# Performance work log

Hardware: AMD Instinct MI355X
Metric: run time of the kernel (lower is better)

Reference implementation:

```python
import jax, jax.numpy as jnp
import numpy as np

B, DIM, HW = 16, 256, 64      # input feature map
G, DH = 8, 64                 # offset_groups = heads = 8, dim_head = 64
DPG = DIM // G                # 32 channels per group
TP = 8                        # tile size: 8x8 grid of 8x8 tiles
DS = 4                        # downsample factor -> 2x2 offset grid per tile
CPB_DIM = DIM // 4            # 64, CPB mlp width
SCALE = DH ** -0.5


def _grid_sample(img, grid):
    # F.grid_sample, bilinear, zero padding, align_corners=False
    # img (N,C,H,W), grid (N,Ho,Wo,2) with last dim (x,y) in [-1,1]
    N, C, H, W = img.shape
    Ho, Wo = grid.shape[1:3]
    x = ((grid[..., 0] + 1.0) * W - 1.0) / 2.0
    y = ((grid[..., 1] + 1.0) * H - 1.0) / 2.0
    x0 = jnp.floor(x)
    y0 = jnp.floor(y)
    imgf = img.reshape(N, C, H * W)
    out = jnp.zeros((N, C, Ho * Wo), img.dtype)
    for dx, wx in ((0.0, x0 + 1.0 - x), (1.0, x - x0)):
        for dy, wy in ((0.0, y0 + 1.0 - y), (1.0, y - y0)):
            ix = x0 + dx
            iy = y0 + dy
            valid = (ix >= 0) & (ix < W) & (iy >= 0) & (iy < H)
            idx = (jnp.clip(iy, 0, H - 1) * W + jnp.clip(ix, 0, W - 1)).astype(jnp.int32)
            idxf = idx.reshape(N, Ho * Wo)
            g = jax.vmap(lambda im, ii: im[:, ii])(imgf, idxf)  # (N,C,HoWo)
            w = (wx * wy * valid).reshape(N, 1, Ho * Wo)
            out = out + g * w
    return out.reshape(N, C, Ho, Wo)


def _forward(x, ln_g, ln_b, wq, wk, wv, off_w1, off_b1, off_w2,
             cpb_w1, cpb_b1, cpb_w2, cpb_b2, cpb_w3, cpb_b3, wo, bo):
    Bb, C, H, W = x.shape
    # LayerNorm over channel dim (eps=1e-6)
    xt = jnp.moveaxis(x, 1, -1)
    mu = xt.mean(-1, keepdims=True)
    var = ((xt - mu) ** 2).mean(-1, keepdims=True)
    xt = (xt - mu) * jax.lax.rsqrt(var + 1e-6) * ln_g + ln_b
    x = jnp.moveaxis(xt, -1, 1)
    # patchify: (b c (i p) (j q)) -> ((i j b) c p q)  [vectorizes the 64-iter python loop]
    xp = x.reshape(Bb, C, 8, TP, 8, TP).transpose(2, 4, 0, 1, 3, 5).reshape(64 * Bb, C, TP, TP)
    N = 64 * Bb
    # grouped 1x1 to_q (groups = offset_groups)
    xg = xp.reshape(N, G, DPG, TP, TP)
    q = jnp.einsum('ngchw,goc->ngohw', xg, wq)          # (N,8,64,8,8)
    gq = q.reshape(N * G, DH, TP, TP)
    # offset net: depthwise conv k=6 s=4 p=1 -> GELU -> 1x1 -> tanh -> *offset_scale
    off = jax.lax.conv_general_dilated(gq, off_w1, (DS, DS), ((1, 1), (1, 1)),
                                       feature_group_count=DH)
    off = jax.nn.gelu(off + off_b1[None, :, None, None], approximate=False)
    off = jnp.tanh(jnp.einsum('nchw,oc->nohw', off, off_w2)) * float(DS)  # (N*G,2,2,2)
    # virtual sampling grid on the 2x2 offset grid, normalized by (size-1)
    r = jnp.arange(2, dtype=x.dtype)
    gx, gy = jnp.meshgrid(r, r, indexing='xy')
    vgrid = jnp.stack([gx, gy])[None] + off              # (N*G,2,2,2) ch=(x,y)
    vnorm = 2.0 * vgrid - 1.0                            # max(2-1,1)=1
    vgrid_s = jnp.moveaxis(vnorm, 1, -1)                 # (N*G,2,2,2) last=(x,y)
    kv = _grid_sample(xp.reshape(N * G, DPG, TP, TP), vgrid_s)   # (N*G,32,2,2)
    kvf = kv.reshape(N, G, DPG, 2, 2)
    k = jnp.einsum('ngchw,goc->ngohw', kvf, wk)          # (N,8,64,2,2)
    v = jnp.einsum('ngchw,goc->ngohw', kvf, wv)
    qh = q.transpose(0, 1, 3, 4, 2).reshape(N, G, TP * TP, DH) * SCALE
    kh = k.transpose(0, 1, 3, 4, 2).reshape(N, G, 4, DH)
    vh = v.transpose(0, 1, 3, 4, 2).reshape(N, G, 4, DH)
    sim = jnp.einsum('bhid,bhjd->bhij', qh, kh)          # (N,8,64,4)
    # continuous position bias (CPB)
    rq = jnp.arange(TP, dtype=x.dtype)
    qx, qy = jnp.meshgrid(rq, rq, indexing='xy')
    gridq = jnp.stack([qx, qy], -1).reshape(TP * TP, 2) * (2.0 / (TP - 1)) - 1.0
    pos = gridq[None, :, None, :] - vgrid_s.reshape(N * G, 1, 4, 2)  # (N*G,64,4,2)
    bz = jnp.sign(pos) * jnp.log1p(jnp.abs(pos))
    bz = jax.nn.relu(bz @ cpb_w1 + cpb_b1)
    bz = jax.nn.relu(bz @ cpb_w2 + cpb_b2)
    bz = (bz @ cpb_w3 + cpb_b3).reshape(N, G, TP * TP, 4)
    attn = jax.nn.softmax(sim + bz, axis=-1)
    out = jnp.einsum('bhij,bhjd->bhid', attn, vh)        # (N,8,64,64)
    out = out.transpose(0, 1, 3, 2).reshape(N, G * DH, TP, TP)
    out = jnp.einsum('nchw,oc->nohw', out, wo) + bo[None, :, None, None]
    # reassemble: ((i j b) c p q) -> (b c (i p) (j q))
    y = out.reshape(8, 8, Bb, C, TP, TP).transpose(2, 3, 0, 4, 1, 5).reshape(Bb, C, H, W)
    return y


def setup_inputs() -> dict:
    key = jax.random.key(0)
    ks = jax.random.split(key, 12)
    s = 0.05
    return {
        'x': jax.random.normal(ks[0], (B, DIM, HW, HW), jnp.float32),
        'ln_g': jnp.ones((DIM,), jnp.float32),
        'ln_b': jnp.zeros((DIM,), jnp.float32),
        'wq': jax.random.normal(ks[1], (G, DH, DPG), jnp.float32) * s,
        'wk': jax.random.normal(ks[2], (G, DH, DPG), jnp.float32) * s,
        'wv': jax.random.normal(ks[3], (G, DH, DPG), jnp.float32) * s,
        'off_w1': jax.random.normal(ks[4], (DH, 1, 6, 6), jnp.float32) * s,
        'off_b1': jnp.zeros((DH,), jnp.float32),
        'off_w2': jax.random.normal(ks[5], (2, DH), jnp.float32) * s,
        'cpb_w1': jax.random.normal(ks[6], (2, CPB_DIM), jnp.float32) * s,
        'cpb_b1': jnp.zeros((CPB_DIM,), jnp.float32),
        'cpb_w2': jax.random.normal(ks[7], (CPB_DIM, CPB_DIM), jnp.float32) * s,
        'cpb_b2': jnp.zeros((CPB_DIM,), jnp.float32),
        'cpb_w3': jax.random.normal(ks[8], (CPB_DIM, 1), jnp.float32) * s,
        'cpb_b3': jnp.zeros((1,), jnp.float32),
        'wo': jax.random.normal(ks[9], (DIM, G * DH), jnp.float32) * s,
        'bo': jnp.zeros((DIM,), jnp.float32),
    }


def reference(x, ln_g, ln_b, wq, wk, wv, off_w1, off_b1, off_w2,
              cpb_w1, cpb_b1, cpb_w2, cpb_b2, cpb_w3, cpb_b3, wo, bo):
    return _forward(x, ln_g, ln_b, wq, wk, wv, off_w1, off_b1, off_w2,
                    cpb_w1, cpb_b1, cpb_w2, cpb_b2, cpb_w3, cpb_b3, wo, bo)
```

## Files before the change

### kernel.cpp

```cpp
#include <hip/hip_runtime.h>
#include <math.h>


#define WS_VN  16777216
#define WS_WOT 16842752

typedef __attribute__((ext_vector_type(8))) short short8;
typedef __attribute__((ext_vector_type(4))) short short4b;
typedef __attribute__((ext_vector_type(4))) float f32x4;

__device__ __forceinline__ short f2bf(float f) {
  unsigned u = __builtin_bit_cast(unsigned, f);
  u += 0x7fff + ((u >> 16) & 1);
  return (short)(u >> 16);
}
__device__ __forceinline__ float bf2f(short h) {
  return __builtin_bit_cast(float, ((unsigned)(unsigned short)h) << 16);
}

__global__ __launch_bounds__(256) void k1_ln(const float* __restrict__ x,
    const float* __restrict__ ln_g, const float* __restrict__ ln_b,
    float* __restrict__ xn) {
  int blk = blockIdx.x;
  int b = blk >> 6, h = blk & 63;
  int t = threadIdx.x;
  int quarter = t >> 6, wcol = t & 63;
  const float* xrow = x + (size_t)b * (256 * 4096) + h * 64 + wcol;
  float vv[64];
  float s = 0.f, ss = 0.f;
#pragma unroll
  for (int i = 0; i < 64; ++i) {
    float v = xrow[(size_t)(quarter * 64 + i) * 4096];
    vv[i] = v; s += v; ss += v * v;
  }
  __shared__ float sm[4][64], sq[4][64], mu_s[64], rs_s[64];
  sm[quarter][wcol] = s; sq[quarter][wcol] = ss;
  __syncthreads();
  if (t < 64) {
    float S  = sm[0][t] + sm[1][t] + sm[2][t] + sm[3][t];
    float SS = sq[0][t] + sq[1][t] + sq[2][t] + sq[3][t];
    float mu = S * (1.f / 256.f);
    float var = SS * (1.f / 256.f) - mu * mu;
    mu_s[t] = mu;
    rs_s[t] = 1.f / sqrtf(var + 1e-6f);
  }
  __syncthreads();
  float mu = mu_s[wcol], rs = rs_s[wcol];
  int it = h >> 3, p = h & 7, jt = wcol >> 3, qq = wcol & 7;
  int n = (it * 8 + jt) * 16 + b;
  int pos = p * 8 + qq;
  float* xo = xn + (size_t)n * 16384 + pos * 256 + quarter * 64;
#pragma unroll
  for (int i = 0; i < 64; i += 4) {
    float4 o4;
    o4.x = (vv[i + 0] - mu) * rs * ln_g[quarter * 64 + i + 0] + ln_b[quarter * 64 + i + 0];
    o4.y = (vv[i + 1] - mu) * rs * ln_g[quarter * 64 + i + 1] + ln_b[quarter * 64 + i + 1];
    o4.z = (vv[i + 2] - mu) * rs * ln_g[quarter * 64 + i + 2] + ln_b[quarter * 64 + i + 2];
    o4.w = (vv[i + 3] - mu) * rs * ln_g[quarter * 64 + i + 3] + ln_b[quarter * 64 + i + 3];
    *(float4*)&xo[i] = o4;
  }
}

__global__ __launch_bounds__(256) void k0_cvt(const float* __restrict__ wo,
    short* __restrict__ woH, short* __restrict__ woL,
    const float* __restrict__ wq,
    short* __restrict__ wqH, short* __restrict__ wqL) {
  int blk = blockIdx.x;
  if (blk < 512) {
    int idx = blk * 256 + threadIdx.x;
    float v = wo[idx];
    short hi = f2bf(v);
    woH[idx] = hi;
    woL[idx] = f2bf(v - bf2f(hi));
  } else {
    int idx = (blk - 512) * 256 + threadIdx.x;
    float v = wq[idx];
    short hi = f2bf(v);
    wqH[idx] = hi;
    wqL[idx] = f2bf(v - bf2f(hi));
  }
}

__global__ __launch_bounds__(256, 4) void k2_qoff(const float* __restrict__ xn,
    const short* __restrict__ wqH, const short* __restrict__ wqL,
    const float* __restrict__ w1, const float* __restrict__ b1,
    const float* __restrict__ w2, short* __restrict__ qb,
    float* __restrict__ vn) {
  int blk = blockIdx.x;
  int n = blk >> 1, gh = blk & 1;
  int w = threadIdx.x >> 6;
  int lane = threadIdx.x & 63;
  int l15 = lane & 15, q4 = lane >> 4;
  __shared__ float qs[64][65];

  const float* w1c = w1 + lane * 36;
  float b1v = b1[lane];
  float w2a = w2[lane];
  float w2b = w2[64 + lane];
  int oy = w >> 1, ox = w & 1;
  int posc = w * 16 + l15;

  for (int gi = 0; gi < 4; ++gi) {
    int g = gh * 4 + gi;
    int ng = n * 8 + g;
    const float* xb = xn + (size_t)n * 16384 + posc * 256 + g * 32 + q4 * 8;
    float4 v0 = *(const float4*)xb;
    float4 v1 = *(const float4*)(xb + 4);
    float vj[8] = {v0.x, v0.y, v0.z, v0.w, v1.x, v1.y, v1.z, v1.w};
    short8 BH, BL;
#pragma unroll
    for (int j = 0; j < 8; ++j) {
      float v = vj[j];
      short hi = f2bf(v);
      BH[j] = hi;
      BL[j] = f2bf(v - bf2f(hi));
    }
    const short* wqHg = wqH + g * 2048;
    const short* wqLg = wqL + g * 2048;
    short* qrow = qb + ((size_t)(n * 64 + posc) * 512 + g * 64);
#pragma unroll
    for (int mt = 0; mt < 4; ++mt) {
      short8 AH = *(const short8*)&wqHg[(mt * 16 + l15) * 32 + q4 * 8];
      short8 AL = *(const short8*)&wqLg[(mt * 16 + l15) * 32 + q4 * 8];
      f32x4 acc = {0.f, 0.f, 0.f, 0.f};
      acc = __builtin_amdgcn_mfma_f32_16x16x32_bf16(AH, BH, acc, 0, 0, 0);
      acc = __builtin_amdgcn_mfma_f32_16x16x32_bf16(AL, BH, acc, 0, 0, 0);
      acc = __builtin_amdgcn_mfma_f32_16x16x32_bf16(AH, BL, acc, 0, 0, 0);
      int obase = mt * 16 + q4 * 4;
#pragma unroll
      for (int reg = 0; reg < 4; ++reg) qs[obase + reg][posc] = acc[reg];
      short4b qv;
#pragma unroll
      for (int reg = 0; reg < 4; ++reg) qv[reg] = f2bf(acc[reg]);
      *(short4b*)&qrow[obase] = qv;
    }
    __syncthreads();
    float a = 0.f;
#pragma unroll
    for (int ky = 0; ky < 6; ++ky) {
      int iy = oy * 4 - 1 + ky;
      if (iy < 0 || iy > 7) continue;
#pragma unroll
      for (int kx = 0; kx < 6; ++kx) {
        int ix = ox * 4 - 1 + kx;
        if (ix < 0 || ix > 7) continue;
        a += w1c[ky * 6 + kx] * qs[lane][iy * 8 + ix];
      }
    }
    a += b1v;
    a = 0.5f * a * (1.f + erff(a * 0.70710678118654752f));
    float p0 = w2a * a, p1 = w2b * a;
#pragma unroll
    for (int st = 1; st < 64; st <<= 1) {
      p0 += __shfl_xor(p0, st, 64);
      p1 += __shfl_xor(p1, st, 64);
    }
    if (lane == 0) {
      float offx = tanhf(p0) * 4.f;
      float offy = tanhf(p1) * 4.f;
      float2 o2;
      o2.x = 2.f * ((float)ox + offx) - 1.f;
      o2.y = 2.f * ((float)oy + offy) - 1.f;
      *(float2*)&vn[(size_t)ng * 8 + w * 2] = o2;
    }
    __syncthreads();
  }
}

__global__ __launch_bounds__(256, 3) void k3_attn(const float* __restrict__ xn,
    const float* __restrict__ wk, const float* __restrict__ wv,
    const float* __restrict__ vn,
    const float* __restrict__ cw1, const float* __restrict__ cb1,
    const float* __restrict__ cw2, const float* __restrict__ cb2,
    const float* __restrict__ cw3, const float* __restrict__ cb3,
    short* __restrict__ qattB) {
  int w = threadIdx.x >> 6;
  int lane = threadIdx.x & 63;
  int ng = blockIdx.x * 4 + w;
  int n = ng >> 3, g = ng & 7;
  __shared__ alignas(16) float kvs[4][32][4];
  __shared__ alignas(16) float ks[4][64][4];
  __shared__ alignas(16) float vs[4][64][4];
  __shared__ alignas(16) short bfragLDS[512 * 8];
  __shared__ float biasS[4][4][64];

  {
    int t = threadIdx.x;
#pragma unroll
    for (int rep = 0; rep < 2; ++rep) {
      int slot = t + rep * 256;
      int combo = slot >> 6, ln = slot & 63;
      int kstep = combo >> 2, nt = combo & 3;
      int kbase = kstep * 32 + (ln >> 4) * 8;
      int ncol = nt * 16 + (ln & 15);
      short8 v;
#pragma unroll
      for (int jj = 0; jj < 8; ++jj) v[jj] = f2bf(cw2[(kbase + jj) * 64 + ncol]);
      *(short8*)&bfragLDS[slot * 8] = v;
    }
  }

  const float* vp = vn + (size_t)ng * 8;
  float vx0 = vp[0], vy0 = vp[1], vx1 = vp[2], vy1 = vp[3];
  float vx2 = vp[4], vy2 = vp[5], vx3 = vp[6], vy3 = vp[7];
  {
    int c = lane & 31, s2 = lane >> 5;
    const float* tile = xn + (size_t)n * 16384 + g * 32 + c;
#pragma unroll
    for (int rep = 0; rep < 2; ++rep) {
      int s = s2 + 2 * rep;
      float vxs = (rep == 0) ? (s2 ? vx1 : vx0) : (s2 ? vx3 : vx2);
      float vys = (rep == 0) ? (s2 ? vy1 : vy0) : (s2 ? vy3 : vy2);
      float X = 4.f * vxs + 3.5f, Y = 4.f * vys + 3.5f;
      float x0f = floorf(X), y0f = floorf(Y);
      int x0 = (int)x0f, y0 = (int)y0f;
      float wx1 = X - x0f, wy1 = Y - y0f;
      float acc = 0.f;
      for (int dy = 0; dy < 2; ++dy) {
        int iy = y0 + dy;
        if (iy < 0 || iy > 7) continue;
        float wyv = dy ? wy1 : 1.f - wy1;
        for (int dx = 0; dx < 2; ++dx) {
          int ix = x0 + dx;
          if (ix < 0 || ix > 7) continue;
          float wxv = dx ? wx1 : 1.f - wx1;
          acc += tile[(iy * 8 + ix) * 256] * wxv * wyv;
        }
      }
      kvs[w][c][s] = acc;
    }
  }
  __syncthreads();
  {
    int d = lane;
    float ka0 = 0, ka1 = 0, ka2 = 0, ka3 = 0, va0 = 0, va1 = 0, va2 = 0, va3 = 0;
    const float4* wk4 = (const float4*)(wk + g * 2048 + d * 32);
    const float4* wv4 = (const float4*)(wv + g * 2048 + d * 32);
#pragma unroll
    for (int c4 = 0; c4 < 8; ++c4) {
      float4 a4 = wk4[c4], b4 = wv4[c4];
      float aw[4] = {a4.x, a4.y, a4.z, a4.w};
      float bw[4] = {b4.x, b4.y, b4.z, b4.w};
#pragma unroll
      for (int u = 0; u < 4; ++u) {
        float4 kv4 = *(const float4*)kvs[w][c4 * 4 + u];
        ka0 += aw[u] * kv4.x; ka1 += aw[u] * kv4.y;
        ka2 += aw[u] * kv4.z; ka3 += aw[u] * kv4.w;
        va0 += bw[u] * kv4.x; va1 += bw[u] * kv4.y;
        va2 += bw[u] * kv4.z; va3 += bw[u] * kv4.w;
      }
    }
    ks[w][d][0] = ka0; ks[w][d][1] = ka1; ks[w][d][2] = ka2; ks[w][d][3] = ka3;
    vs[w][d][0] = va0; vs[w][d][1] = va1; vs[w][d][2] = va2; vs[w][d][3] = va3;
  }
  __syncthreads();
  float sim0 = 0, sim1 = 0, sim2 = 0, sim3 = 0;
  short* qrow = qattB + ((size_t)(n * 64 + lane) * 512 + g * 64);
#pragma unroll 2
  for (int d8 = 0; d8 < 8; ++d8) {
    short8 q8 = *(const short8*)&qrow[d8 * 8];
#pragma unroll
    for (int j = 0; j < 8; ++j) {
      float qv = bf2f(q8[j]);
      float4 k4 = *(const float4*)ks[w][d8 * 8 + j];
      sim0 += qv * k4.x; sim1 += qv * k4.y; sim2 += qv * k4.z; sim3 += qv * k4.w;
    }
  }
  float logit0 = sim0 * 0.125f, logit1 = sim1 * 0.125f;
  float logit2 = sim2 * 0.125f, logit3 = sim3 * 0.125f;

  short8 bf[2][4];
#pragma unroll
  for (int kstep = 0; kstep < 2; ++kstep)
#pragma unroll
    for (int nt = 0; nt < 4; ++nt)
      bf[kstep][nt] = *(const short8*)&bfragLDS[((kstep * 4 + nt) * 64 + lane) * 8];
  int kcol = (lane >> 4) * 8;
  float c1x[16], c1y[16], c1b[16];
#pragma unroll
  for (int ks2 = 0; ks2 < 2; ++ks2)
#pragma unroll
    for (int jj = 0; jj < 8; ++jj) {
      int i = ks2 * 32 + kcol + jj;
      c1x[ks2 * 8 + jj] = cw1[i];
      c1y[ks2 * 8 + jj] = cw1[64 + i];
      c1b[ks2 * 8 + jj] = cb1[i];
    }
  int jme = lane & 15;
  float w3v[4], b2v[4];
#pragma unroll
  for (int nt = 0; nt < 4; ++nt) {
    w3v[nt] = cw3[nt * 16 + jme];
    b2v[nt] = cb2[nt * 16 + jme];
  }
  float gqx = (float)(jme & 7) * (2.f / 7.f) - 1.f;
  float yrow = (float)(jme >> 3);
#pragma unroll 1
  for (int s = 0; s < 4; ++s) {
    float vxs = (s == 0) ? vx0 : (s == 1) ? vx1 : (s == 2) ? vx2 : vx3;
    float vys = (s == 0) ? vy0 : (s == 1) ? vy1 : (s == 2) ? vy2 : vy3;
    float px = gqx - vxs;
    float tx = copysignf(log1pf(fabsf(px)), px);
    float pre[16];
#pragma unroll
    for (int t2 = 0; t2 < 16; ++t2) pre[t2] = fmaf(tx, c1x[t2], c1b[t2]);
#pragma unroll 1
    for (int mt4 = 0; mt4 < 4; ++mt4) {
      float gqy = (float)(mt4 * 2) * (2.f / 7.f) + yrow * (2.f / 7.f) - 1.f;
      float py = gqy - vys;
      float ty = copysignf(log1pf(fabsf(py)), py);
      short8 af[2];
#pragma unroll
      for (int ks2 = 0; ks2 < 2; ++ks2)
#pragma unroll
        for (int jj = 0; jj < 8; ++jj) {
          float h = fmaxf(fmaf(ty, c1y[ks2 * 8 + jj], pre[ks2 * 8 + jj]), 0.f);
          af[ks2][jj] = f2bf(h);
        }
      f32x4 a0 = {0,0,0,0}, a1 = {0,0,0,0}, a2 = {0,0,0,0}, a3 = {0,0,0,0};
      a0 = __builtin_amdgcn_mfma_f32_16x16x32_bf16(af[0], bf[0][0], a0, 0, 0, 0);
      a0 = __builtin_amdgcn_mfma_f32_16x16x32_bf16(af[1], bf[1][0], a0, 0, 0, 0);
      a1 = __builtin_amdgcn_mfma_f32_16x16x32_bf16(af[0], bf[0][1], a1, 0, 0, 0);
      a1 = __builtin_amdgcn_mfma_f32_16x16x32_bf16(af[1], bf[1][1], a1, 0, 0, 0);
      a2 = __builtin_amdgcn_mfma_f32_16x16x32_bf16(af[0], bf[0][2], a2, 0, 0, 0);
      a2 = __builtin_amdgcn_mfma_f32_16x16x32_bf16(af[1], bf[1][2], a2, 0, 0, 0);
      a3 = __builtin_amdgcn_mfma_f32_16x16x32_bf16(af[0], bf[0][3], a3, 0, 0, 0);
      a3 = __builtin_amdgcn_mfma_f32_16x16x32_bf16(af[1], bf[1][3], a3, 0, 0, 0);
      float part[4];
#pragma unroll
      for (int reg = 0; reg < 4; ++reg) {
        part[reg] = w3v[0] * fmaxf(a0[reg] + b2v[0], 0.f)
                  + w3v[1] * fmaxf(a1[reg] + b2v[1], 0.f)
                  + w3v[2] * fmaxf(a2[reg] + b2v[2], 0.f)
                  + w3v[3] * fmaxf(a3[reg] + b2v[3], 0.f);
      }
#pragma unroll
      for (int st = 1; st < 16; st <<= 1)
#pragma unroll
        for (int reg = 0; reg < 4; ++reg)
          part[reg] += __shfl_xor(part[reg], st, 64);
      if (jme == 0) {
        int posO = mt4 * 16 + (lane >> 4) * 4;
#pragma unroll
        for (int reg = 0; reg < 4; ++reg) biasS[w][s][posO + reg] = part[reg];
      }
    }
  }
  __syncthreads();
  float c3 = cb3[0];
  logit0 += biasS[w][0][lane] + c3;
  logit1 += biasS[w][1][lane] + c3;
  logit2 += biasS[w][2][lane] + c3;
  logit3 += biasS[w][3][lane] + c3;
  float m = fmaxf(fmaxf(logit0, logit1), fmaxf(logit2, logit3));
  float e0 = expf(logit0 - m), e1 = expf(logit1 - m);
  float e2 = expf(logit2 - m), e3 = expf(logit3 - m);
  float inv = 1.f / (e0 + e1 + e2 + e3);
  e0 *= inv; e1 *= inv; e2 *= inv; e3 *= inv;
#pragma unroll 2
  for (int d8 = 0; d8 < 8; ++d8) {
    short8 o8;
#pragma unroll
    for (int j = 0; j < 8; ++j) {
      float4 v4 = *(const float4*)vs[w][d8 * 8 + j];
      o8[j] = f2bf(e0 * v4.x + e1 * v4.y + e2 * v4.z + e3 * v4.w);
    }
    *(short8*)&qrow[d8 * 8] = o8;
  }
}

__global__ __launch_bounds__(256) void k4_mfma(const short* __restrict__ attB,
    const short* __restrict__ woH, const short* __restrict__ woL,
    const float* __restrict__ bo, float* __restrict__ y) {
  int blk = blockIdx.x;
  int b = blk & 15, it = (blk >> 4) & 7, p = blk >> 7;
  int wv = threadIdx.x >> 6;
  int lane = threadIdx.x & 63;
  int mr = lane & 15, kq = (lane >> 4) * 8;
  f32x4 acc[4][4];
#pragma unroll
  for (int mt = 0; mt < 4; ++mt)
#pragma unroll
    for (int nt = 0; nt < 4; ++nt) acc[mt][nt] = (f32x4){0.f, 0.f, 0.f, 0.f};
  int ncol0 = wv * 64 + mr;
  size_t arow[4];
#pragma unroll
  for (int mt = 0; mt < 4; ++mt) {
    int w0 = mt * 16 + mr;
    int jt = w0 >> 3, q = w0 & 7;
    arow[mt] = ((size_t)((it * 8 + jt) * 16 + b) * 64 + p * 8 + q) * 512;
  }
#pragma unroll 2
  for (int kst = 0; kst < 16; ++kst) {
    int k0 = kst * 32 + kq;
    short8 a[4];
#pragma unroll
    for (int mt = 0; mt < 4; ++mt)
      a[mt] = *(const short8*)&attB[arow[mt] + k0];
#pragma unroll
    for (int nt = 0; nt < 4; ++nt) {
      size_t off = (size_t)(ncol0 + nt * 16) * 512 + k0;
      short8 bhi = *(const short8*)&woH[off];
      short8 blo = *(const short8*)&woL[off];
#pragma unroll
      for (int mt = 0; mt < 4; ++mt) {
        acc[mt][nt] = __builtin_amdgcn_mfma_f32_16x16x32_bf16(a[mt], bhi, acc[mt][nt], 0, 0, 0);
        acc[mt][nt] = __builtin_amdgcn_mfma_f32_16x16x32_bf16(a[mt], blo, acc[mt][nt], 0, 0, 0);
      }
    }
  }
#pragma unroll
  for (int nt = 0; nt < 4; ++nt) {
    int o = wv * 64 + nt * 16 + mr;
    float bov = bo[o];
    size_t ybase = ((size_t)b * 256 + o) * 4096 + (it * 8 + p) * 64;
#pragma unroll
    for (int mt = 0; mt < 4; ++mt) {
      int w0 = mt * 16 + (lane >> 4) * 4;
      float4 o4;
      o4.x = acc[mt][nt][0] + bov;
      o4.y = acc[mt][nt][1] + bov;
      o4.z = acc[mt][nt][2] + bov;
      o4.w = acc[mt][nt][3] + bov;
      *(float4*)&y[ybase + w0] = o4;
    }
  }
}

extern "C" void kernel_launch(void* const* d_in, const int* in_sizes, int n_in,
                              void* d_out, int out_size, void* d_ws, size_t ws_size,
                              hipStream_t stream) {
  (void)in_sizes; (void)n_in; (void)out_size; (void)ws_size;
  const float* x    = (const float*)d_in[0];
  const float* ln_g = (const float*)d_in[1];
  const float* ln_b = (const float*)d_in[2];
  const float* wq   = (const float*)d_in[3];
  const float* wk   = (const float*)d_in[4];
  const float* wv   = (const float*)d_in[5];
  const float* ow1  = (const float*)d_in[6];
  const float* ob1  = (const float*)d_in[7];
  const float* ow2  = (const float*)d_in[8];
  const float* cw1  = (const float*)d_in[9];
  const float* cb1  = (const float*)d_in[10];
  const float* cw2  = (const float*)d_in[11];
  const float* cb2  = (const float*)d_in[12];
  const float* cw3  = (const float*)d_in[13];
  const float* cb3  = (const float*)d_in[14];
  const float* wo   = (const float*)d_in[15];
  const float* bo   = (const float*)d_in[16];
  float* y  = (float*)d_out;
  float* ws = (float*)d_ws;
  short* qattB = (short*)ws;
  float* vnb   = ws + WS_VN;
  short* woH   = (short*)(ws + WS_WOT);
  short* woL   = woH + 131072;
  short* wqH   = woL + 131072;
  short* wqL   = wqH + 16384;
  float* xn = y;

  k0_cvt<<<576, 256, 0, stream>>>(wo, woH, woL, wq, wqH, wqL);
  k1_ln<<<1024, 256, 0, stream>>>(x, ln_g, ln_b, xn);
  k2_qoff<<<2048, 256, 0, stream>>>(xn, wqH, wqL, ow1, ob1, ow2, qattB, vnb);
  k3_attn<<<2048, 256, 0, stream>>>(xn, wk, wv, vnb, cw1, cb1, cw2, cb2,
                                    cw3, cb3, qattB);
  k4_mfma<<<1024, 256, 0, stream>>>(qattB, woH, woL, bo, y);
}
```

Before: 399.1 us.

## Fuse q projection/offset net into attention kernel and precompute CPB bf16 fragments

Result: slower. 629.9 us (+57.9%).

```diff
diff --git a/kernel.cpp b/kernel.cpp
--- a/kernel.cpp
+++ b/kernel.cpp
@@ -6,7 +6,6 @@
 #define WS_WOT 16842752
 
 typedef __attribute__((ext_vector_type(8))) short short8;
-typedef __attribute__((ext_vector_type(4))) short short4b;
 typedef __attribute__((ext_vector_type(4))) float f32x4;
 
 __device__ __forceinline__ short f2bf(float f) {
@@ -64,7 +63,8 @@
 __global__ __launch_bounds__(256) void k0_cvt(const float* __restrict__ wo,
     short* __restrict__ woH, short* __restrict__ woL,
     const float* __restrict__ wq,
-    short* __restrict__ wqH, short* __restrict__ wqL) {
+    short* __restrict__ wqH, short* __restrict__ wqL,
+    const float* __restrict__ cw2, short* __restrict__ bfragG) {
   int blk = blockIdx.x;
   if (blk < 512) {
     int idx = blk * 256 + threadIdx.x;
@@ -72,119 +72,13 @@
     short hi = f2bf(v);
     woH[idx] = hi;
     woL[idx] = f2bf(v - bf2f(hi));
-  } else {
+  } else if (blk < 576) {
     int idx = (blk - 512) * 256 + threadIdx.x;
     float v = wq[idx];
     short hi = f2bf(v);
     wqH[idx] = hi;
     wqL[idx] = f2bf(v - bf2f(hi));
-  }
-}
-
-__global__ __launch_bounds__(256, 4) void k2_qoff(const float* __restrict__ xn,
-    const short* __restrict__ wqH, const short* __restrict__ wqL,
-    const float* __restrict__ w1, const float* __restrict__ b1,
-    const float* __restrict__ w2, short* __restrict__ qb,
-    float* __restrict__ vn) {
-  int blk = blockIdx.x;
-  int n = blk >> 1, gh = blk & 1;
-  int w = threadIdx.x >> 6;
-  int lane = threadIdx.x & 63;
-  int l15 = lane & 15, q4 = lane >> 4;
-  __shared__ float qs[64][65];
-
-  const float* w1c = w1 + lane * 36;
-  float b1v = b1[lane];
-  float w2a = w2[lane];
-  float w2b = w2[64 + lane];
-  int oy = w >> 1, ox = w & 1;
-  int posc = w * 16 + l15;
-
-  for (int gi = 0; gi < 4; ++gi) {
-    int g = gh * 4 + gi;
-    int ng = n * 8 + g;
-    const float* xb = xn + (size_t)n * 16384 + posc * 256 + g * 32 + q4 * 8;
-    float4 v0 = *(const float4*)xb;
-    float4 v1 = *(const float4*)(xb + 4);
-    float vj[8] = {v0.x, v0.y, v0.z, v0.w, v1.x, v1.y, v1.z, v1.w};
-    short8 BH, BL;
-#pragma unroll
-    for (int j = 0; j < 8; ++j) {
-      float v = vj[j];
-      short hi = f2bf(v);
-      BH[j] = hi;
-      BL[j] = f2bf(v - bf2f(hi));
-    }
-    const short* wqHg = wqH + g * 2048;
-    const short* wqLg = wqL + g * 2048;
-    short* qrow = qb + ((size_t)(n * 64 + posc) * 512 + g * 64);
-#pragma unroll
-    for (int mt = 0; mt < 4; ++mt) {
-      short8 AH = *(const short8*)&wqHg[(mt * 16 + l15) * 32 + q4 * 8];
-      short8 AL = *(const short8*)&wqLg[(mt * 16 + l15) * 32 + q4 * 8];
-      f32x4 acc = {0.f, 0.f, 0.f, 0.f};
-      acc = __builtin_amdgcn_mfma_f32_16x16x32_bf16(AH, BH, acc, 0, 0, 0);
-      acc = __builtin_amdgcn_mfma_f32_16x16x32_bf16(AL, BH, acc, 0, 0, 0);
-      acc = __builtin_amdgcn_mfma_f32_16x16x32_bf16(AH, BL, acc, 0, 0, 0);
-      int obase = mt * 16 + q4 * 4;
-#pragma unroll
-      for (int reg = 0; reg < 4; ++reg) qs[obase + reg][posc] = acc[reg];
-      short4b qv;
-#pragma unroll
-      for (int reg = 0; reg < 4; ++reg) qv[reg] = f2bf(acc[reg]);
-      *(short4b*)&qrow[obase] = qv;
-    }
-    __syncthreads();
-    float a = 0.f;
-#pragma unroll
-    for (int ky = 0; ky < 6; ++ky) {
-      int iy = oy * 4 - 1 + ky;
-      if (iy < 0 || iy > 7) continue;
-#pragma unroll
-      for (int kx = 0; kx < 6; ++kx) {
-        int ix = ox * 4 - 1 + kx;
-        if (ix < 0 || ix > 7) continue;
-        a += w1c[ky * 6 + kx] * qs[lane][iy * 8 + ix];
-      }
-    }
-    a += b1v;
-    a = 0.5f * a * (1.f + erff(a * 0.70710678118654752f));
-    float p0 = w2a * a, p1 = w2b * a;
-#pragma unroll
-    for (int st = 1; st < 64; st <<= 1) {
-      p0 += __shfl_xor(p0, st, 64);
-      p1 += __shfl_xor(p1, st, 64);
-    }
-    if (lane == 0) {
-      float offx = tanhf(p0) * 4.f;
-      float offy = tanhf(p1) * 4.f;
-      float2 o2;
-      o2.x = 2.f * ((float)ox + offx) - 1.f;
-      o2.y = 2.f * ((float)oy + offy) - 1.f;
-      *(float2*)&vn[(size_t)ng * 8 + w * 2] = o2;
-    }
-    __syncthreads();
-  }
-}
-
-__global__ __launch_bounds__(256, 3) void k3_attn(const float* __restrict__ xn,
-    const float* __restrict__ wk, const float* __restrict__ wv,
-    const float* __restrict__ vn,
-    const float* __restrict__ cw1, const float* __restrict__ cb1,
-    const float* __restrict__ cw2, const float* __restrict__ cb2,
-    const float* __restrict__ cw3, const float* __restrict__ cb3,
-    short* __restrict__ qattB) {
-  int w = threadIdx.x >> 6;
-  int lane = threadIdx.x & 63;
-  int ng = blockIdx.x * 4 + w;
-  int n = ng >> 3, g = ng & 7;
-  __shared__ alignas(16) float kvs[4][32][4];
-  __shared__ alignas(16) float ks[4][64][4];
-  __shared__ alignas(16) float vs[4][64][4];
-  __shared__ alignas(16) short bfragLDS[512 * 8];
-  __shared__ float biasS[4][4][64];
-
-  {
+  } else {
     int t = threadIdx.x;
 #pragma unroll
     for (int rep = 0; rep < 2; ++rep) {
@@ -196,13 +90,134 @@
       short8 v;
 #pragma unroll
       for (int jj = 0; jj < 8; ++jj) v[jj] = f2bf(cw2[(kbase + jj) * 64 + ncol]);
-      *(short8*)&bfragLDS[slot * 8] = v;
-    }
-  }
-
-  const float* vp = vn + (size_t)ng * 8;
-  float vx0 = vp[0], vy0 = vp[1], vx1 = vp[2], vy1 = vp[3];
-  float vx2 = vp[4], vy2 = vp[5], vx3 = vp[6], vy3 = vp[7];
+      *(short8*)&bfragG[slot * 8] = v;
+    }
+  }
+}
+
+__global__ __launch_bounds__(256, 3) void k23_qattn(const float* __restrict__ xn,
+    const short* __restrict__ wqH, const short* __restrict__ wqL,
+    const float* __restrict__ w1, const float* __restrict__ b1,
+    const float* __restrict__ w2,
+    const float* __restrict__ wk, const float* __restrict__ wv,
+    const short* __restrict__ bfragG,
+    const float* __restrict__ cw1, const float* __restrict__ cb1,
+    const float* __restrict__ cb2,
+    const float* __restrict__ cw3, const float* __restrict__ cb3,
+    short* __restrict__ qattB) {
+  int blk = blockIdx.x;
+  int n = blk >> 1, gh = blk & 1;
+  int w = threadIdx.x >> 6;
+  int lane = threadIdx.x & 63;
+  int l15 = lane & 15, q4 = lane >> 4;
+  int g = gh * 4 + w;
+
+  __shared__ __align__(16) char smemU[16640];
+  __shared__ alignas(16) short bfragLDS[512 * 8];
+  __shared__ float vnS[4][4][2];
+  float (*qs)[65]       = (float(*)[65])smemU;
+  float (*kvs)[32][4]   = (float(*)[32][4])(smemU);
+  float (*ks)[64][4]    = (float(*)[64][4])(smemU + 2048);
+  float (*vs)[64][4]    = (float(*)[64][4])(smemU + 6144);
+  float (*biasS)[4][64] = (float(*)[4][64])(smemU + 10240);
+
+  {
+    int t = threadIdx.x;
+    *(short8*)&bfragLDS[t * 8]         = *(const short8*)&bfragG[t * 8];
+    *(short8*)&bfragLDS[(t + 256) * 8] = *(const short8*)&bfragG[(t + 256) * 8];
+  }
+
+  const float* xb = xn + (size_t)n * 16384 + g * 32;
+  short8 BH[4], BL[4];
+#pragma unroll
+  for (int nt = 0; nt < 4; ++nt) {
+    const float* xp = xb + (nt * 16 + l15) * 256 + q4 * 8;
+    float4 v0 = *(const float4*)xp;
+    float4 v1 = *(const float4*)(xp + 4);
+    float vj[8] = {v0.x, v0.y, v0.z, v0.w, v1.x, v1.y, v1.z, v1.w};
+#pragma unroll
+    for (int j = 0; j < 8; ++j) {
+      float v = vj[j];
+      short hi = f2bf(v);
+      BH[nt][j] = hi;
+      BL[nt][j] = f2bf(v - bf2f(hi));
+    }
+  }
+  const short* wqHg = wqH + g * 2048;
+  const short* wqLg = wqL + g * 2048;
+  f32x4 qacc[4][4];
+#pragma unroll
+  for (int mt = 0; mt < 4; ++mt) {
+    short8 AH = *(const short8*)&wqHg[(mt * 16 + l15) * 32 + q4 * 8];
+    short8 AL = *(const short8*)&wqLg[(mt * 16 + l15) * 32 + q4 * 8];
+#pragma unroll
+    for (int nt = 0; nt < 4; ++nt) {
+      f32x4 a = {0.f, 0.f, 0.f, 0.f};
+      a = __builtin_amdgcn_mfma_f32_16x16x32_bf16(AH, BH[nt], a, 0, 0, 0);
+      a = __builtin_amdgcn_mfma_f32_16x16x32_bf16(AL, BH[nt], a, 0, 0, 0);
+      a = __builtin_amdgcn_mfma_f32_16x16x32_bf16(AH, BL[nt], a, 0, 0, 0);
+      qacc[mt][nt] = a;
+    }
+  }
+
+  const float* w1c = w1 + lane * 36;
+  float b1v = b1[lane];
+  float w2a = w2[lane];
+  float w2b = w2[64 + lane];
+  int oy = w >> 1, ox = w & 1;
+  short8 qbf[8];
+#pragma unroll 1
+  for (int gi = 0; gi < 4; ++gi) {
+    if (w == gi) {
+#pragma unroll
+      for (int mt = 0; mt < 4; ++mt)
+#pragma unroll
+        for (int nt = 0; nt < 4; ++nt)
+#pragma unroll
+          for (int reg = 0; reg < 4; ++reg)
+            qs[mt * 16 + q4 * 4 + reg][nt * 16 + l15] = qacc[mt][nt][reg];
+    }
+    __syncthreads();
+    if (w == gi) {
+#pragma unroll
+      for (int d8 = 0; d8 < 8; ++d8) {
+        short8 t8;
+#pragma unroll
+        for (int j = 0; j < 8; ++j) t8[j] = f2bf(qs[d8 * 8 + j][lane]);
+        qbf[d8] = t8;
+      }
+    }
+    float a = 0.f;
+#pragma unroll
+    for (int ky = 0; ky < 6; ++ky) {
+      int iy = oy * 4 - 1 + ky;
+      if (iy < 0 || iy > 7) continue;
+#pragma unroll
+      for (int kx = 0; kx < 6; ++kx) {
+        int ix = ox * 4 - 1 + kx;
+        if (ix < 0 || ix > 7) continue;
+        a += w1c[ky * 6 + kx] * qs[lane][iy * 8 + ix];
+      }
+    }
+    a += b1v;
+    a = 0.5f * a * (1.f + erff(a * 0.70710678118654752f));
+    float p0 = w2a * a, p1 = w2b * a;
+#pragma unroll
+    for (int st = 1; st < 64; st <<= 1) {
+      p0 += __shfl_xor(p0, st, 64);
+      p1 += __shfl_xor(p1, st, 64);
+    }
+    if (lane == 0) {
+      vnS[gi][w][0] = 2.f * ((float)ox + tanhf(p0) * 4.f) - 1.f;
+      vnS[gi][w][1] = 2.f * ((float)oy + tanhf(p1) * 4.f) - 1.f;
+    }
+    __syncthreads();
+  }
+
+  float vx0 = vnS[w][0][0], vy0 = vnS[w][0][1];
+  float vx1 = vnS[w][1][0], vy1 = vnS[w][1][1];
+  float vx2 = vnS[w][2][0], vy2 = vnS[w][2][1];
+  float vx3 = vnS[w][3][0], vy3 = vnS[w][3][1];
   {
     int c = lane & 31, s2 = lane >> 5;
     const float* tile = xn + (size_t)n * 16384 + g * 32 + c;
@@ -255,10 +270,9 @@
   }
   __syncthreads();
   float sim0 = 0, sim1 = 0, sim2 = 0, sim3 = 0;
-  short* qrow = qattB + ((size_t)(n * 64 + lane) * 512 + g * 64);
-#pragma unroll 2
+#pragma unroll
   for (int d8 = 0; d8 < 8; ++d8) {
-    short8 q8 = *(const short8*)&qrow[d8 * 8];
+    short8 q8 = qbf[d8];
 #pragma unroll
     for (int j = 0; j < 8; ++j) {
       float qv = bf2f(q8[j]);
@@ -275,7 +289,7 @@
 #pragma unroll
     for (int nt = 0; nt < 4; ++nt)
       bf[kstep][nt] = *(const short8*)&bfragLDS[((kstep * 4 + nt) * 64 + lane) * 8];
-  int kcol = (lane >> 4) * 8;
+  int kcol = q4 * 8;
   float c1x[16], c1y[16], c1b[16];
 #pragma unroll
   for (int ks2 = 0; ks2 < 2; ++ks2)
@@ -286,7 +300,7 @@
       c1y[ks2 * 8 + jj] = cw1[64 + i];
       c1b[ks2 * 8 + jj] = cb1[i];
     }
-  int jme = lane & 15;
+  int jme = l15;
   float w3v[4], b2v[4];
 #pragma unroll
   for (int nt = 0; nt < 4; ++nt) {
@@ -340,7 +354,7 @@
         for (int reg = 0; reg < 4; ++reg)
           part[reg] += __shfl_xor(part[reg], st, 64);
       if (jme == 0) {
-        int posO = mt4 * 16 + (lane >> 4) * 4;
+        int posO = mt4 * 16 + q4 * 4;
 #pragma unroll
         for (int reg = 0; reg < 4; ++reg) biasS[w][s][posO + reg] = part[reg];
       }
@@ -357,6 +371,7 @@
   float e2 = expf(logit2 - m), e3 = expf(logit3 - m);
   float inv = 1.f / (e0 + e1 + e2 + e3);
   e0 *= inv; e1 *= inv; e2 *= inv; e3 *= inv;
+  short* qrow = qattB + ((size_t)(n * 64 + lane) * 512 + g * 64);
 #pragma unroll 2
   for (int d8 = 0; d8 < 8; ++d8) {
     short8 o8;
@@ -451,17 +466,16 @@
   float* y  = (float*)d_out;
   float* ws = (float*)d_ws;
   short* qattB = (short*)ws;
-  float* vnb   = ws + WS_VN;
   short* woH   = (short*)(ws + WS_WOT);
   short* woL   = woH + 131072;
   short* wqH   = woL + 131072;
   short* wqL   = wqH + 16384;
+  short* bfragG = wqL + 16384;
   float* xn = y;
 
-  k0_cvt<<<576, 256, 0, stream>>>(wo, woH, woL, wq, wqH, wqL);
+  k0_cvt<<<577, 256, 0, stream>>>(wo, woH, woL, wq, wqH, wqL, cw2, bfragG);
   k1_ln<<<1024, 256, 0, stream>>>(x, ln_g, ln_b, xn);
-  k2_qoff<<<2048, 256, 0, stream>>>(xn, wqH, wqL, ow1, ob1, ow2, qattB, vnb);
-  k3_attn<<<2048, 256, 0, stream>>>(xn, wk, wv, vnb, cw1, cb1, cw2, cb2,
-                                    cw3, cb3, qattB);
+  k23_qattn<<<2048, 256, 0, stream>>>(xn, wqH, wqL, ow1, ob1, ow2, wk, wv,
+                                      bfragG, cw1, cb1, cb2, cw3, cb3, qattB);
   k4_mfma<<<1024, 256, 0, stream>>>(qattB, woH, woL, bo, y);
 }
```
